# Optimization experiments

Hardware: AMD Instinct MI355X
Metric: run time of the kernel (lower is better)

## Reference

```python
import jax, jax.numpy as jnp
import numpy as np

N_NODES = 100000
N_EDGES = 1600000
N_GRAPHS = 100
DIMS = [128, 128, 118, 103, 5]  # in_feats, h, h-10, h-25, num_classes


def setup_inputs() -> dict:
    key = jax.random.key(0)
    ks = jax.random.split(key, 16)
    inp = {
        "in_feat": jax.random.normal(ks[0], (N_NODES, DIMS[0]), dtype=jnp.float32),
        "src": jax.random.randint(ks[1], (N_EDGES,), 0, N_NODES, dtype=jnp.int32),
        "dst": jax.random.randint(ks[2], (N_EDGES,), 0, N_NODES, dtype=jnp.int32),
        "graph_ids": (jnp.arange(N_NODES, dtype=jnp.int32) // (N_NODES // N_GRAPHS)),
    }
    # SAGEConv params: fc_self (no bias), fc_neigh (no bias), shared bias
    for l in range(4):
        din, dout = DIMS[l], DIMS[l + 1]
        inp[f"ws{l+1}"] = jax.random.normal(ks[3 + 3 * l], (din, dout), dtype=jnp.float32) * 0.05
        inp[f"wn{l+1}"] = jax.random.normal(ks[4 + 3 * l], (din, dout), dtype=jnp.float32) * 0.05
        inp[f"b{l+1}"] = jnp.zeros((dout,), dtype=jnp.float32)
    return inp


def reference(in_feat, src, dst, graph_ids,
              ws1, wn1, b1, ws2, wn2, b2, ws3, wn3, b3, ws4, wn4, b4):
    N = in_feat.shape[0]
    # in-degree per dst node, clamped to 1 (DGL: degs.clamp(min=1))
    deg = jnp.clip(jax.ops.segment_sum(jnp.ones((src.shape[0],), in_feat.dtype), dst,
                                       num_segments=N), 1.0, None)

    def sage(h, ws, wn, b):
        # mean-aggregate neighbor features: gather over src, scatter-add to dst
        agg = jax.ops.segment_sum(h[src], dst, num_segments=N) / deg[:, None]
        return h @ ws + agg @ wn + b

    h = jax.nn.relu(sage(in_feat, ws1, wn1, b1))
    h = jax.nn.relu(sage(h, ws2, wn2, b2))
    h = jax.nn.relu(sage(h, ws3, wn3, b3))
    h = sage(h, ws4, wn4, b4)

    # dgl.mean_nodes: per-graph mean pooling over nodes
    ones = jnp.ones((N,), h.dtype)
    cnt = jax.ops.segment_sum(ones, graph_ids, num_segments=N_GRAPHS)
    pooled = jax.ops.segment_sum(h, graph_ids, num_segments=N_GRAPHS) / cnt[:, None]
    return pooled
```

## Files before the change

kernel.cpp:

```cpp
#include <hip/hip_runtime.h>
#include <cstdint>
#include <cstddef>

typedef unsigned int uint32;
typedef unsigned short ushort16;
typedef __attribute__((ext_vector_type(8))) short short8;
typedef __attribute__((ext_vector_type(4))) float floatx4;

__device__ __forceinline__ ushort16 f2bf(float f) {
    uint32 u = __builtin_bit_cast(uint32, f);
    uint32 r = (u + 0x7fffu + ((u >> 16) & 1u)) >> 16;
    return (ushort16)r;
}
__device__ __forceinline__ float bf2f(ushort16 h) {
    uint32 u = ((uint32)h) << 16;
    return __builtin_bit_cast(float, u);
}

#define PBS 4096


__global__ __launch_bounds__(256) void bucket_hist_kernel(
    const int* __restrict__ dst, int* __restrict__ bcnt, int E, int NBUCK) {
    __shared__ int l[512];
    int t = threadIdx.x;
    for (int b = t; b < NBUCK; b += 256) l[b] = 0;
    __syncthreads();
    int e0 = blockIdx.x * PBS;
    int e1 = e0 + PBS; if (e1 > E) e1 = E;
    for (int j = e0 + t; j < e1; j += 256)
        atomicAdd(&l[dst[j] >> 8], 1);
    __syncthreads();
    for (int b = t; b < NBUCK; b += 256) {
        int c = l[b];
        if (c) atomicAdd(&bcnt[b], c);
    }
}

__global__ __launch_bounds__(256) void bucket_scan_kernel(
    const int* __restrict__ bcnt, int* __restrict__ bucketOff,
    int* __restrict__ cursorA, int NBUCK, int E) {
    __shared__ int a[512], b[512];
    int t = threadIdx.x;
    a[t] = (t < NBUCK) ? bcnt[t] : 0;
    a[t + 256] = (t + 256 < NBUCK) ? bcnt[t + 256] : 0;
    __syncthreads();
    int* cur = a; int* nxt = b;
    for (int o = 1; o < 512; o <<= 1) {
#pragma unroll
        for (int i = t; i < 512; i += 256)
            nxt[i] = cur[i] + ((i >= o) ? cur[i - o] : 0);
        __syncthreads();
        int* tmp = cur; cur = nxt; nxt = tmp;
    }
#pragma unroll
    for (int i = t; i < 512; i += 256) {
        if (i <= NBUCK) {
            int off = (i == 0) ? 0 : cur[i - 1];
            bucketOff[i] = off;
            if (i < NBUCK) cursorA[i] = off;
        }
    }
    if (t == 0) bucketOff[NBUCK] = E;
}

__global__ __launch_bounds__(256) void bucket_partition_kernel(
    const int* __restrict__ src, const int* __restrict__ dst,
    int* __restrict__ cursorA, uint32* __restrict__ ebuf, int E, int NBUCK) {
    __shared__ int lbase[512];
    int tid = threadIdx.x;
    for (int b = tid; b < NBUCK; b += 256) lbase[b] = 0;
    __syncthreads();
    int e0 = blockIdx.x * PBS;
    int e1 = e0 + PBS; if (e1 > E) e1 = E;
    for (int j = e0 + tid; j < e1; j += 256)
        atomicAdd(&lbase[dst[j] >> 8], 1);
    __syncthreads();
    for (int b = tid; b < NBUCK; b += 256) {
        int c = lbase[b];
        lbase[b] = c ? atomicAdd(&cursorA[b], c) : 0;
    }
    __syncthreads();
    for (int j = e0 + tid; j < e1; j += 256) {
        int d = dst[j];
        int p = atomicAdd(&lbase[d >> 8], 1);
        ebuf[p] = ((uint32)src[j] << 8) | (uint32)(d & 255);
    }
}

__global__ __launch_bounds__(256) void bucket_build_kernel(
    const uint32* __restrict__ ebuf, const int* __restrict__ bucketOff,
    int* __restrict__ row_ptr, float* __restrict__ degf,
    int* __restrict__ csr, int N, int E) {
    __shared__ int ldeg[256];
    __shared__ int lscan[256];
    __shared__ int lcur[256];
    int b = blockIdx.x, t = threadIdx.x;
    int n0 = b << 8;
    int s = bucketOff[b], e = bucketOff[b + 1];
    ldeg[t] = 0;
    __syncthreads();
    for (int j = s + t; j < e; j += 256)
        atomicAdd(&ldeg[ebuf[j] & 255u], 1);
    __syncthreads();
    int v = ldeg[t];
    lscan[t] = v;
    __syncthreads();
    for (int off = 1; off < 256; off <<= 1) {
        int x = (t >= off) ? lscan[t - off] : 0;
        __syncthreads();
        lscan[t] += x;
        __syncthreads();
    }
    int excl = lscan[t] - v;
    int node = n0 + t;
    if (node < N) {
        row_ptr[node] = s + excl;
        degf[node] = (float)(v > 0 ? v : 1);
    }
    lcur[t] = s + excl;
    __syncthreads();
    for (int j = s + t; j < e; j += 256) {
        uint32 en = ebuf[j];
        int p = atomicAdd(&lcur[en & 255u], 1);
        csr[p] = (int)(en >> 8);
    }
    if (b == 0 && t == 0) row_ptr[N] = E;
}

__global__ void conv_bf16_kernel(const float* __restrict__ x, ushort16* __restrict__ y, int n8) {
    int i = blockIdx.x * blockDim.x + threadIdx.x;
    if (i >= n8) return;
    const float4 a = *(const float4*)(x + (size_t)i * 8);
    const float4 b = *(const float4*)(x + (size_t)i * 8 + 4);
    uint4 o;
    o.x = (uint32)f2bf(a.x) | ((uint32)f2bf(a.y) << 16);
    o.y = (uint32)f2bf(a.z) | ((uint32)f2bf(a.w) << 16);
    o.z = (uint32)f2bf(b.x) | ((uint32)f2bf(b.y) << 16);
    o.w = (uint32)f2bf(b.z) | ((uint32)f2bf(b.w) << 16);
    *(uint4*)(y + (size_t)i * 8) = o;
}

__global__ void prep_w_all_kernel(
    const float* __restrict__ W0s, const float* __restrict__ W0n,
    const float* __restrict__ W1s, const float* __restrict__ W1n,
    const float* __restrict__ W2s, const float* __restrict__ W2n,
    ushort16* __restrict__ Whi, ushort16* __restrict__ Wlo) {
    int mat = blockIdx.x >> 6;
    int idx = (blockIdx.x & 63) * 256 + threadIdx.x;
    const float* Wt[6] = {W0s, W0n, W1s, W1n, W2s, W2n};
    const int Kt[6] = {128, 128, 128, 128, 118, 118};
    const int Mt[6] = {128, 128, 118, 118, 103, 103};
    int n = idx >> 7, k = idx & 127;
    int K = Kt[mat], M = Mt[mat];
    float w = (k < K && n < M) ? Wt[mat][(size_t)k * M + n] : 0.f;
    ushort16 h = f2bf(w);
    float lo = w - bf2f(h);
    Whi[(size_t)mat * 16384 + idx] = h;
    Wlo[(size_t)mat * 16384 + idx] = f2bf(lo);
}

template<int UNROLL>
__global__ __launch_bounds__(256) void aggregate_pre_kernel(
    const ushort16* __restrict__ h,
    const int* __restrict__ row_ptr, const int* __restrict__ csr,
    const float* __restrict__ degf, ushort16* __restrict__ aggH, int N) {
    int wid = threadIdx.x >> 6;
    int lane = threadIdx.x & 63;
    int node = blockIdx.x * 4 + wid;
    if (node >= N) return;
    int s = row_ptr[node], e = row_ptr[node + 1];
    int c = lane & 15;
    int eo = lane >> 4;
    float aLo[4] = {}, aHi[4] = {};
    int j = s + eo;
    for (; j + (UNROLL - 1) * 4 < e; j += UNROLL * 4) {
        uint4 v[UNROLL];
#pragma unroll
        for (int u = 0; u < UNROLL; ++u) {
            int src_n = csr[j + u * 4];
            v[u] = *(const uint4*)(h + ((size_t)src_n << 7) + (c << 3));
        }
#pragma unroll
        for (int u = 0; u < UNROLL; ++u) {
            uint32 w[4] = {v[u].x, v[u].y, v[u].z, v[u].w};
#pragma unroll
            for (int p = 0; p < 4; ++p) {
                aLo[p] += __builtin_bit_cast(float, w[p] << 16);
                aHi[p] += __builtin_bit_cast(float, w[p] & 0xffff0000u);
            }
        }
    }
    for (; j < e; j += 4) {
        int src_n = csr[j];
        uint4 v = *(const uint4*)(h + ((size_t)src_n << 7) + (c << 3));
        uint32 w[4] = {v.x, v.y, v.z, v.w};
#pragma unroll
        for (int p = 0; p < 4; ++p) {
            aLo[p] += __builtin_bit_cast(float, w[p] << 16);
            aHi[p] += __builtin_bit_cast(float, w[p] & 0xffff0000u);
        }
    }
#pragma unroll
    for (int m = 16; m < 64; m <<= 1) {
#pragma unroll
        for (int p = 0; p < 4; ++p) {
            aLo[p] += __shfl_xor(aLo[p], m, 64);
            aHi[p] += __shfl_xor(aHi[p], m, 64);
        }
    }
    if (lane < 16) {
        float inv = 1.f / degf[node];
        uint4 ov;
        ov.x = (uint32)f2bf(aLo[0] * inv) | ((uint32)f2bf(aHi[0] * inv) << 16);
        ov.y = (uint32)f2bf(aLo[1] * inv) | ((uint32)f2bf(aHi[1] * inv) << 16);
        ov.z = (uint32)f2bf(aLo[2] * inv) | ((uint32)f2bf(aHi[2] * inv) << 16);
        ov.w = (uint32)f2bf(aLo[3] * inv) | ((uint32)f2bf(aHi[3] * inv) << 16);
        *(uint4*)(aggH + ((size_t)node << 7) + (c << 3)) = ov;
    }
}

#define RS 40
__global__ __launch_bounds__(256) void mfma_fused_kernel(
    const ushort16* __restrict__ A, const ushort16* __restrict__ G,
    const ushort16* __restrict__ Whi, const ushort16* __restrict__ Wlo,
    const float* __restrict__ bias,
    ushort16* __restrict__ Out, int N, int M) {
    __shared__ ushort16 Bs[4][128 * RS];
    const int tid = threadIdx.x;
    const int wave = tid >> 6;
    const int lane = tid & 63;
    const int quad = lane >> 4;
    const int m16 = lane & 15;
    const ushort16* Wg[4] = {Whi, Wlo, Whi + 16384, Wlo + 16384};

    floatx4 acc[8] = {};

    int rowA = blockIdx.x * 64 + wave * 16 + m16;
    if (rowA >= N) rowA = N - 1;
    const ushort16* Arow = A + (size_t)rowA * 128;
    const ushort16* Grow = G + (size_t)rowA * 128;

    const int sn = tid >> 1, shalf = tid & 1;
    for (int k0 = 0; k0 < 128; k0 += 32) {
#pragma unroll
        for (int mat = 0; mat < 4; ++mat) {
            const ushort16* g = Wg[mat] + (size_t)sn * 128 + k0 + shalf * 16;
            uint4 v0 = *(const uint4*)(g);
            uint4 v1 = *(const uint4*)(g + 8);
            ushort16* d = &Bs[mat][sn * RS + shalf * 16];
            *(uint4*)(d) = v0;
            *(uint4*)(d + 8) = v1;
        }
        __syncthreads();
        short8 af = *(const short8*)(Arow + k0 + quad * 8);
        short8 gf = *(const short8*)(Grow + k0 + quad * 8);
#pragma unroll
        for (int t = 0; t < 8; ++t) {
            int nb = t * 16 + m16;
            short8 bsh = *(const short8*)(&Bs[0][nb * RS + quad * 8]);
            short8 bsl = *(const short8*)(&Bs[1][nb * RS + quad * 8]);
            short8 bnh = *(const short8*)(&Bs[2][nb * RS + quad * 8]);
            short8 bnl = *(const short8*)(&Bs[3][nb * RS + quad * 8]);
            acc[t] = __builtin_amdgcn_mfma_f32_16x16x32_bf16(af, bsh, acc[t], 0, 0, 0);
            acc[t] = __builtin_amdgcn_mfma_f32_16x16x32_bf16(gf, bnh, acc[t], 0, 0, 0);
            acc[t] = __builtin_amdgcn_mfma_f32_16x16x32_bf16(af, bsl, acc[t], 0, 0, 0);
            acc[t] = __builtin_amdgcn_mfma_f32_16x16x32_bf16(gf, bnl, acc[t], 0, 0, 0);
        }
        __syncthreads();
    }

    int rowBase = blockIdx.x * 64 + wave * 16 + quad * 4;
#pragma unroll
    for (int t = 0; t < 8; ++t) {
        int col = t * 16 + m16;
        bool inc = (col < M);
        float b = inc ? bias[col] : 0.f;
#pragma unroll
        for (int r = 0; r < 4; ++r) {
            int row = rowBase + r;
            if (row >= N) continue;
            float v = inc ? fmaxf(acc[t][r] + b, 0.f) : 0.f;
            Out[(size_t)row * 128 + col] = f2bf(v);
        }
    }
}

__global__ __launch_bounds__(256) void gemm4_kernel(
    const ushort16* __restrict__ A, const float* __restrict__ ws,
    const float* __restrict__ wn, const float* __restrict__ b4,
    float* __restrict__ Cs, float* __restrict__ Cn, int N, int K, int M) {
    __shared__ float Wsh[520], Wnh[520];
    int tid = threadIdx.x;
    for (int i = tid; i < K * M; i += 256) { Wsh[i] = ws[i]; Wnh[i] = wn[i]; }
    __syncthreads();
    int node = blockIdx.x * 256 + tid;
    if (node >= N) return;
    const ushort16* row = A + ((size_t)node << 7);
    float s[5] = {}, n[5] = {};
    for (int c8 = 0; c8 * 8 < K; ++c8) {
        uint4 v = *(const uint4*)(row + c8 * 8);
        uint32 w[4] = {v.x, v.y, v.z, v.w};
#pragma unroll
        for (int j = 0; j < 8; ++j) {
            int k = c8 * 8 + j;
            if (k < K) {
                float a = (j & 1) ? __builtin_bit_cast(float, w[j >> 1] & 0xffff0000u)
                                  : __builtin_bit_cast(float, w[j >> 1] << 16);
#pragma unroll
                for (int m = 0; m < 5; ++m) {
                    s[m] += a * Wsh[k * 5 + m];
                    n[m] += a * Wnh[k * 5 + m];
                }
            }
        }
    }
    size_t o = (size_t)node * 8;
#pragma unroll
    for (int m = 0; m < 5; ++m) {
        Cs[o + m] = s[m] + b4[m];
        Cn[o + m] = n[m];
    }
#pragma unroll
    for (int m = 5; m < 8; ++m) { Cs[o + m] = 0.f; Cn[o + m] = 0.f; }
}

template<int CPW, int UNROLL, int SLOG>
__global__ __launch_bounds__(256) void aggregate_fp32_kernel(
    const float* __restrict__ hs, const float* __restrict__ hn,
    const int* __restrict__ row_ptr, const int* __restrict__ csr,
    const float* __restrict__ degf, float* __restrict__ out, int N) {
    constexpr int EPI = 64 / CPW;
    int wid = threadIdx.x >> 6;
    int lane = threadIdx.x & 63;
    int node = blockIdx.x * 4 + wid;
    if (node >= N) return;
    int s = row_ptr[node], e = row_ptr[node + 1];
    int c = lane & (CPW - 1);
    int eo = lane / CPW;
    float4 acc = make_float4(0.f, 0.f, 0.f, 0.f);
    int j = s + eo;
    for (; j + (UNROLL - 1) * EPI < e; j += UNROLL * EPI) {
        float4 v[UNROLL];
#pragma unroll
        for (int u = 0; u < UNROLL; ++u) {
            int src_n = csr[j + u * EPI];
            v[u] = *(const float4*)(hn + ((size_t)src_n << SLOG) + (c << 2));
        }
#pragma unroll
        for (int u = 0; u < UNROLL; ++u) {
            acc.x += v[u].x; acc.y += v[u].y; acc.z += v[u].z; acc.w += v[u].w;
        }
    }
    for (; j < e; j += EPI) {
        int src_n = csr[j];
        float4 v = *(const float4*)(hn + ((size_t)src_n << SLOG) + (c << 2));
        acc.x += v.x; acc.y += v.y; acc.z += v.z; acc.w += v.w;
    }
#pragma unroll
    for (int m = CPW; m < 64; m <<= 1) {
        acc.x += __shfl_xor(acc.x, m, 64);
        acc.y += __shfl_xor(acc.y, m, 64);
        acc.z += __shfl_xor(acc.z, m, 64);
        acc.w += __shfl_xor(acc.w, m, 64);
    }
    if (lane < CPW) {
        float d = 1.f / degf[node];
        size_t o = ((size_t)node << SLOG) + (lane << 2);
        float4 hv = *(const float4*)(hs + o);
        float4 r;
        r.x = hv.x + acc.x * d;
        r.y = hv.y + acc.y * d;
        r.z = hv.z + acc.z * d;
        r.w = hv.w + acc.w * d;
        *(float4*)(out + o) = r;
    }
}

__global__ __launch_bounds__(256) void pool_kernel(
    const float* __restrict__ h, float* __restrict__ out, int npg) {
    __shared__ float sh[4][5];
    int g = blockIdx.x;
    int t = threadIdx.x;
    float acc[5] = {0.f, 0.f, 0.f, 0.f, 0.f};
    int base = g * npg;
    for (int i = t; i < npg; i += 256) {
        const float* r = h + ((size_t)(base + i) << 3);
#pragma unroll
        for (int f = 0; f < 5; ++f) acc[f] += r[f];
    }
#pragma unroll
    for (int off = 32; off > 0; off >>= 1) {
#pragma unroll
        for (int f = 0; f < 5; ++f) acc[f] += __shfl_down(acc[f], off, 64);
    }
    int wid = t >> 6, lane = t & 63;
    if (lane == 0) {
#pragma unroll
        for (int f = 0; f < 5; ++f) sh[wid][f] = acc[f];
    }
    __syncthreads();
    if (t == 0) {
        float inv = 1.f / (float)npg;
#pragma unroll
        for (int f = 0; f < 5; ++f)
            out[g * 5 + f] = (sh[0][f] + sh[1][f] + sh[2][f] + sh[3][f]) * inv;
    }
}

extern "C" void kernel_launch(void* const* d_in, const int* in_sizes, int n_in,
                              void* d_out, int out_size, void* d_ws, size_t ws_size,
                              hipStream_t stream) {
    const float* in_feat = (const float*)d_in[0];
    const int* src = (const int*)d_in[1];
    const int* dst = (const int*)d_in[2];
    const int DIMS[5] = {128, 128, 118, 103, 5};
    const int N = in_sizes[0] / 128;
    const int E = in_sizes[1];
    const int G = out_size / 5;
    const int NBUCK = (N + 255) >> 8;

    char* base = (char*)d_ws;
    size_t off = 0;
    auto carve = [&](size_t bytes) -> void* {
        off = (off + 255) & ~(size_t)255;
        void* p = base + off;
        off += bytes;
        return p;
    };
    int* bcnt = (int*)carve((size_t)NBUCK * 4);
    int* bucketOff = (int*)carve((size_t)(NBUCK + 1) * 4);
    int* cursorA = (int*)carve((size_t)NBUCK * 4);
    int* row_ptr = (int*)carve((size_t)(N + 1) * 4);
    float* degf = (float*)carve((size_t)N * 4);
    uint32* ebuf = (uint32*)carve((size_t)E * 4);
    int* csr = (int*)carve((size_t)E * 4);
    ushort16* buf0 = (ushort16*)carve((size_t)(N + 64) * 128 * 2);
    ushort16* buf1 = (ushort16*)carve((size_t)(N + 64) * 128 * 2);
    ushort16* aggH = (ushort16*)carve((size_t)(N + 64) * 128 * 2);
    ushort16* Whi = (ushort16*)carve((size_t)6 * 16384 * 2);
    ushort16* Wlo = (ushort16*)carve((size_t)6 * 16384 * 2);
    float* Cs4 = (float*)carve((size_t)N * 8 * 4);
    float* Cn4 = (float*)carve((size_t)N * 8 * 4);
    float* out4 = (float*)carve((size_t)N * 8 * 4);
    (void)n_in; (void)ws_size;

    hipMemsetAsync(bcnt, 0, (size_t)NBUCK * 4, stream);
    bucket_hist_kernel<<<(E + PBS - 1) / PBS, 256, 0, stream>>>(dst, bcnt, E, NBUCK);
    bucket_scan_kernel<<<1, 256, 0, stream>>>(bcnt, bucketOff, cursorA, NBUCK, E);
    bucket_partition_kernel<<<(E + PBS - 1) / PBS, 256, 0, stream>>>(
        src, dst, cursorA, ebuf, E, NBUCK);
    bucket_build_kernel<<<NBUCK, 256, 0, stream>>>(
        ebuf, bucketOff, row_ptr, degf, csr, N, E);

    int n8 = N * 16;
    conv_bf16_kernel<<<(n8 + 255) / 256, 256, 0, stream>>>(in_feat, buf0, n8);
    prep_w_all_kernel<<<6 * 64, 256, 0, stream>>>(
        (const float*)d_in[4], (const float*)d_in[5],
        (const float*)d_in[7], (const float*)d_in[8],
        (const float*)d_in[10], (const float*)d_in[11],
        Whi, Wlo);

    ushort16* hb[4] = {buf0, buf1, buf0, buf1};
    int gblocks = (N + 63) / 64;
    for (int l = 0; l < 3; ++l) {
        int M = DIMS[l + 1];
        const float* b = (const float*)d_in[6 + 3 * l];
        aggregate_pre_kernel<4><<<(N + 3) / 4, 256, 0, stream>>>(
            hb[l], row_ptr, csr, degf, aggH, N);
        mfma_fused_kernel<<<gblocks, 256, 0, stream>>>(
            hb[l], aggH, Whi + (size_t)l * 2 * 16384, Wlo + (size_t)l * 2 * 16384,
            b, hb[l + 1], N, M);
    }

    gemm4_kernel<<<(N + 255) / 256, 256, 0, stream>>>(
        hb[3], (const float*)d_in[13], (const float*)d_in[14], (const float*)d_in[15],
        Cs4, Cn4, N, DIMS[3], DIMS[4]);
    aggregate_fp32_kernel<2, 1, 3><<<(N + 3) / 4, 256, 0, stream>>>(
        Cs4, Cn4, row_ptr, csr, degf, out4, N);
    pool_kernel<<<G, 256, 0, stream>>>(out4, (float*)d_out, N / G);
}
```

Baseline: 520.2 us.

## Drop LDS weight staging and tile 64 rows per wave in fused MFMA GEMM

Restructures the fused layer GEMM so each wave keeps a 64-row tile of A and aggregated features in registers, and reads weight fragments straight from global memory (L2-cached) instead of staging them in shared memory behind barriers. Each weight fragment is now reused across four row sub-tiles, which removes the __syncthreads and the LDS traffic. Each block now covers 256 rows, so there are fewer blocks. The cost is much higher register pressure (32 short8 input fragments held per lane), which lowers occupancy, plus uncoalesced global weight loads.

```diff
diff --git a/kernel.cpp b/kernel.cpp
--- a/kernel.cpp
+++ b/kernel.cpp
@@ -18,7 +18,6 @@
 }
 
 #define PBS 4096
-
 
 __global__ __launch_bounds__(256) void bucket_hist_kernel(
     const int* __restrict__ dst, int* __restrict__ bcnt, int E, int NBUCK) {
@@ -220,68 +219,70 @@
     }
 }
 
-#define RS 40
 __global__ __launch_bounds__(256) void mfma_fused_kernel(
     const ushort16* __restrict__ A, const ushort16* __restrict__ G,
     const ushort16* __restrict__ Whi, const ushort16* __restrict__ Wlo,
     const float* __restrict__ bias,
     ushort16* __restrict__ Out, int N, int M) {
-    __shared__ ushort16 Bs[4][128 * RS];
     const int tid = threadIdx.x;
     const int wave = tid >> 6;
     const int lane = tid & 63;
     const int quad = lane >> 4;
     const int m16 = lane & 15;
-    const ushort16* Wg[4] = {Whi, Wlo, Whi + 16384, Wlo + 16384};
-
-    floatx4 acc[8] = {};
-
-    int rowA = blockIdx.x * 64 + wave * 16 + m16;
-    if (rowA >= N) rowA = N - 1;
-    const ushort16* Arow = A + (size_t)rowA * 128;
-    const ushort16* Grow = G + (size_t)rowA * 128;
-
-    const int sn = tid >> 1, shalf = tid & 1;
-    for (int k0 = 0; k0 < 128; k0 += 32) {
-#pragma unroll
-        for (int mat = 0; mat < 4; ++mat) {
-            const ushort16* g = Wg[mat] + (size_t)sn * 128 + k0 + shalf * 16;
-            uint4 v0 = *(const uint4*)(g);
-            uint4 v1 = *(const uint4*)(g + 8);
-            ushort16* d = &Bs[mat][sn * RS + shalf * 16];
-            *(uint4*)(d) = v0;
-            *(uint4*)(d + 8) = v1;
-        }
-        __syncthreads();
-        short8 af = *(const short8*)(Arow + k0 + quad * 8);
-        short8 gf = *(const short8*)(Grow + k0 + quad * 8);
-#pragma unroll
-        for (int t = 0; t < 8; ++t) {
-            int nb = t * 16 + m16;
-            short8 bsh = *(const short8*)(&Bs[0][nb * RS + quad * 8]);
-            short8 bsl = *(const short8*)(&Bs[1][nb * RS + quad * 8]);
-            short8 bnh = *(const short8*)(&Bs[2][nb * RS + quad * 8]);
-            short8 bnl = *(const short8*)(&Bs[3][nb * RS + quad * 8]);
-            acc[t] = __builtin_amdgcn_mfma_f32_16x16x32_bf16(af, bsh, acc[t], 0, 0, 0);
-            acc[t] = __builtin_amdgcn_mfma_f32_16x16x32_bf16(gf, bnh, acc[t], 0, 0, 0);
-            acc[t] = __builtin_amdgcn_mfma_f32_16x16x32_bf16(af, bsl, acc[t], 0, 0, 0);
-            acc[t] = __builtin_amdgcn_mfma_f32_16x16x32_bf16(gf, bnl, acc[t], 0, 0, 0);
-        }
-        __syncthreads();
-    }
-
-    int rowBase = blockIdx.x * 64 + wave * 16 + quad * 4;
+    const ushort16* Ws_hi = Whi;
+    const ushort16* Ws_lo = Wlo;
+    const ushort16* Wn_hi = Whi + 16384;
+    const ushort16* Wn_lo = Wlo + 16384;
+
+    const int tilebase = (blockIdx.x * 4 + wave) * 64;
+
+    short8 af[4][4], gf[4][4];
+#pragma unroll
+    for (int i = 0; i < 4; ++i) {
+        int row = tilebase + i * 16 + m16;
+        if (row >= N) row = N - 1;
+        const ushort16* Ar = A + (size_t)row * 128 + quad * 8;
+        const ushort16* Gr = G + (size_t)row * 128 + quad * 8;
+#pragma unroll
+        for (int k = 0; k < 4; ++k) {
+            af[i][k] = *(const short8*)(Ar + k * 32);
+            gf[i][k] = *(const short8*)(Gr + k * 32);
+        }
+    }
+
 #pragma unroll
     for (int t = 0; t < 8; ++t) {
-        int col = t * 16 + m16;
-        bool inc = (col < M);
-        float b = inc ? bias[col] : 0.f;
-#pragma unroll
-        for (int r = 0; r < 4; ++r) {
-            int row = rowBase + r;
-            if (row >= N) continue;
-            float v = inc ? fmaxf(acc[t][r] + b, 0.f) : 0.f;
-            Out[(size_t)row * 128 + col] = f2bf(v);
+        floatx4 acc[4] = {};
+        const int nb = t * 16 + m16;
+        const size_t boff = (size_t)nb * 128 + quad * 8;
+#pragma unroll
+        for (int k = 0; k < 4; ++k) {
+            short8 bsh = *(const short8*)(Ws_hi + boff + k * 32);
+            short8 bnh = *(const short8*)(Wn_hi + boff + k * 32);
+            short8 bsl = *(const short8*)(Ws_lo + boff + k * 32);
+            short8 bnl = *(const short8*)(Wn_lo + boff + k * 32);
+#pragma unroll
+            for (int i = 0; i < 4; ++i) {
+                acc[i] = __builtin_amdgcn_mfma_f32_16x16x32_bf16(af[i][k], bsh, acc[i], 0, 0, 0);
+                acc[i] = __builtin_amdgcn_mfma_f32_16x16x32_bf16(gf[i][k], bnh, acc[i], 0, 0, 0);
+                acc[i] = __builtin_amdgcn_mfma_f32_16x16x32_bf16(af[i][k], bsl, acc[i], 0, 0, 0);
+                acc[i] = __builtin_amdgcn_mfma_f32_16x16x32_bf16(gf[i][k], bnl, acc[i], 0, 0, 0);
+            }
+        }
+        const int colt = t * 16 + m16;
+        const bool inc = (colt < M);
+        const float b = inc ? bias[colt] : 0.f;
+#pragma unroll
+        for (int i = 0; i < 4; ++i) {
+            int rowBase = tilebase + i * 16 + quad * 4;
+#pragma unroll
+            for (int r = 0; r < 4; ++r) {
+                int row = rowBase + r;
+                if (row < N) {
+                    float v = inc ? fmaxf(acc[i][r] + b, 0.f) : 0.f;
+                    Out[(size_t)row * 128 + colt] = f2bf(v);
+                }
+            }
         }
     }
 }
@@ -435,9 +436,9 @@
     float* degf = (float*)carve((size_t)N * 4);
     uint32* ebuf = (uint32*)carve((size_t)E * 4);
     int* csr = (int*)carve((size_t)E * 4);
-    ushort16* buf0 = (ushort16*)carve((size_t)(N + 64) * 128 * 2);
-    ushort16* buf1 = (ushort16*)carve((size_t)(N + 64) * 128 * 2);
-    ushort16* aggH = (ushort16*)carve((size_t)(N + 64) * 128 * 2);
+    ushort16* buf0 = (ushort16*)carve((size_t)(N + 256) * 128 * 2);
+    ushort16* buf1 = (ushort16*)carve((size_t)(N + 256) * 128 * 2);
+    ushort16* aggH = (ushort16*)carve((size_t)(N + 256) * 128 * 2);
     ushort16* Whi = (ushort16*)carve((size_t)6 * 16384 * 2);
     ushort16* Wlo = (ushort16*)carve((size_t)6 * 16384 * 2);
     float* Cs4 = (float*)carve((size_t)N * 8 * 4);
@@ -462,7 +463,7 @@
         Whi, Wlo);
 
     ushort16* hb[4] = {buf0, buf1, buf0, buf1};
-    int gblocks = (N + 63) / 64;
+    int gblocks = (N + 255) / 256;
     for (int l = 0; l < 3; ++l) {
         int M = DIMS[l + 1];
         const float* b = (const float*)d_in[6 + 3 * l];
```

Result: slower. 564.2 us (+8.5%).

## Fuse neighbor aggregation into the MFMA layer GEMM via LDS

Applied to the files above, without the earlier changes.

Merges the per-layer mean-aggregation kernel into the MFMA GEMM kernel. Each 64-row block first gathers and averages neighbor features for its rows into shared memory, then runs the dual-weight bf16 MFMA using the LDS aggregate instead of a global aggH buffer. This removes one launch per layer and the global write and read of the aggregated features. In exchange, only 4 waves per block do the gather, 16 nodes each in sequence, so latency hiding may drop, and the extra LDS cuts occupancy. A third ping-pong buffer is added so a layer never reads and writes the same buffer.

```diff
diff --git a/kernel.cpp b/kernel.cpp
--- a/kernel.cpp
+++ b/kernel.cpp
@@ -18,7 +18,6 @@
 }
 
 #define PBS 4096
-
 
 __global__ __launch_bounds__(256) void bucket_hist_kernel(
     const int* __restrict__ dst, int* __restrict__ bcnt, int E, int NBUCK) {
@@ -160,86 +159,88 @@
     Wlo[(size_t)mat * 16384 + idx] = f2bf(lo);
 }
 
-template<int UNROLL>
-__global__ __launch_bounds__(256) void aggregate_pre_kernel(
-    const ushort16* __restrict__ h,
+#define RS 40
+#define GHS 136
+__global__ __launch_bounds__(256) void layer_fused_kernel(
+    const ushort16* __restrict__ A,
     const int* __restrict__ row_ptr, const int* __restrict__ csr,
-    const float* __restrict__ degf, ushort16* __restrict__ aggH, int N) {
-    int wid = threadIdx.x >> 6;
-    int lane = threadIdx.x & 63;
-    int node = blockIdx.x * 4 + wid;
-    if (node >= N) return;
-    int s = row_ptr[node], e = row_ptr[node + 1];
-    int c = lane & 15;
-    int eo = lane >> 4;
-    float aLo[4] = {}, aHi[4] = {};
-    int j = s + eo;
-    for (; j + (UNROLL - 1) * 4 < e; j += UNROLL * 4) {
-        uint4 v[UNROLL];
-#pragma unroll
-        for (int u = 0; u < UNROLL; ++u) {
-            int src_n = csr[j + u * 4];
-            v[u] = *(const uint4*)(h + ((size_t)src_n << 7) + (c << 3));
-        }
-#pragma unroll
-        for (int u = 0; u < UNROLL; ++u) {
-            uint32 w[4] = {v[u].x, v[u].y, v[u].z, v[u].w};
-#pragma unroll
-            for (int p = 0; p < 4; ++p) {
-                aLo[p] += __builtin_bit_cast(float, w[p] << 16);
-                aHi[p] += __builtin_bit_cast(float, w[p] & 0xffff0000u);
-            }
-        }
-    }
-    for (; j < e; j += 4) {
-        int src_n = csr[j];
-        uint4 v = *(const uint4*)(h + ((size_t)src_n << 7) + (c << 3));
-        uint32 w[4] = {v.x, v.y, v.z, v.w};
-#pragma unroll
-        for (int p = 0; p < 4; ++p) {
-            aLo[p] += __builtin_bit_cast(float, w[p] << 16);
-            aHi[p] += __builtin_bit_cast(float, w[p] & 0xffff0000u);
-        }
-    }
-#pragma unroll
-    for (int m = 16; m < 64; m <<= 1) {
-#pragma unroll
-        for (int p = 0; p < 4; ++p) {
-            aLo[p] += __shfl_xor(aLo[p], m, 64);
-            aHi[p] += __shfl_xor(aHi[p], m, 64);
-        }
-    }
-    if (lane < 16) {
-        float inv = 1.f / degf[node];
-        uint4 ov;
-        ov.x = (uint32)f2bf(aLo[0] * inv) | ((uint32)f2bf(aHi[0] * inv) << 16);
-        ov.y = (uint32)f2bf(aLo[1] * inv) | ((uint32)f2bf(aHi[1] * inv) << 16);
-        ov.z = (uint32)f2bf(aLo[2] * inv) | ((uint32)f2bf(aHi[2] * inv) << 16);
-        ov.w = (uint32)f2bf(aLo[3] * inv) | ((uint32)f2bf(aHi[3] * inv) << 16);
-        *(uint4*)(aggH + ((size_t)node << 7) + (c << 3)) = ov;
-    }
-}
-
-#define RS 40
-__global__ __launch_bounds__(256) void mfma_fused_kernel(
-    const ushort16* __restrict__ A, const ushort16* __restrict__ G,
+    const float* __restrict__ degf,
     const ushort16* __restrict__ Whi, const ushort16* __restrict__ Wlo,
     const float* __restrict__ bias,
     ushort16* __restrict__ Out, int N, int M) {
     __shared__ ushort16 Bs[4][128 * RS];
+    __shared__ ushort16 Gs[64 * GHS];
     const int tid = threadIdx.x;
     const int wave = tid >> 6;
     const int lane = tid & 63;
     const int quad = lane >> 4;
     const int m16 = lane & 15;
+    const int blockbase = blockIdx.x * 64;
+
+    {
+        const int c = lane & 15;
+        const int eo = lane >> 4;
+        for (int i = 0; i < 16; ++i) {
+            int lrow = wave * 16 + i;
+            int node = blockbase + lrow;
+            if (node >= N) break;
+            int s = row_ptr[node], e = row_ptr[node + 1];
+            float aLo[4] = {}, aHi[4] = {};
+            int j = s + eo;
+            for (; j + 12 < e; j += 16) {
+                uint4 v[4];
+#pragma unroll
+                for (int u = 0; u < 4; ++u) {
+                    int src_n = csr[j + u * 4];
+                    v[u] = *(const uint4*)(A + ((size_t)src_n << 7) + (c << 3));
+                }
+#pragma unroll
+                for (int u = 0; u < 4; ++u) {
+                    uint32 w[4] = {v[u].x, v[u].y, v[u].z, v[u].w};
+#pragma unroll
+                    for (int p = 0; p < 4; ++p) {
+                        aLo[p] += __builtin_bit_cast(float, w[p] << 16);
+                        aHi[p] += __builtin_bit_cast(float, w[p] & 0xffff0000u);
+                    }
+                }
+            }
+            for (; j < e; j += 4) {
+                int src_n = csr[j];
+                uint4 v = *(const uint4*)(A + ((size_t)src_n << 7) + (c << 3));
+                uint32 w[4] = {v.x, v.y, v.z, v.w};
+#pragma unroll
+                for (int p = 0; p < 4; ++p) {
+                    aLo[p] += __builtin_bit_cast(float, w[p] << 16);
+                    aHi[p] += __builtin_bit_cast(float, w[p] & 0xffff0000u);
+                }
+            }
+#pragma unroll
+            for (int m = 16; m < 64; m <<= 1) {
+#pragma unroll
+                for (int p = 0; p < 4; ++p) {
+                    aLo[p] += __shfl_xor(aLo[p], m, 64);
+                    aHi[p] += __shfl_xor(aHi[p], m, 64);
+                }
+            }
+            if (lane < 16) {
+                float inv = 1.f / degf[node];
+                uint4 ov;
+                ov.x = (uint32)f2bf(aLo[0] * inv) | ((uint32)f2bf(aHi[0] * inv) << 16);
+                ov.y = (uint32)f2bf(aLo[1] * inv) | ((uint32)f2bf(aHi[1] * inv) << 16);
+                ov.z = (uint32)f2bf(aLo[2] * inv) | ((uint32)f2bf(aHi[2] * inv) << 16);
+                ov.w = (uint32)f2bf(aLo[3] * inv) | ((uint32)f2bf(aHi[3] * inv) << 16);
+                *(uint4*)(&Gs[lrow * GHS + (c << 3)]) = ov;
+            }
+        }
+    }
+    __syncthreads();
+
     const ushort16* Wg[4] = {Whi, Wlo, Whi + 16384, Wlo + 16384};
-
     floatx4 acc[8] = {};
-
-    int rowA = blockIdx.x * 64 + wave * 16 + m16;
+    int rowA = blockbase + wave * 16 + m16;
     if (rowA >= N) rowA = N - 1;
     const ushort16* Arow = A + (size_t)rowA * 128;
-    const ushort16* Grow = G + (size_t)rowA * 128;
+    const ushort16* Glds = Gs + (wave * 16 + m16) * GHS;
 
     const int sn = tid >> 1, shalf = tid & 1;
     for (int k0 = 0; k0 < 128; k0 += 32) {
@@ -252,9 +253,9 @@
             *(uint4*)(d) = v0;
             *(uint4*)(d + 8) = v1;
         }
+        short8 af = *(const short8*)(Arow + k0 + quad * 8);
         __syncthreads();
-        short8 af = *(const short8*)(Arow + k0 + quad * 8);
-        short8 gf = *(const short8*)(Grow + k0 + quad * 8);
+        short8 gf = *(const short8*)(Glds + k0 + quad * 8);
 #pragma unroll
         for (int t = 0; t < 8; ++t) {
             int nb = t * 16 + m16;
@@ -270,18 +271,19 @@
         __syncthreads();
     }
 
-    int rowBase = blockIdx.x * 64 + wave * 16 + quad * 4;
+    int rowBase = blockbase + wave * 16 + quad * 4;
 #pragma unroll
     for (int t = 0; t < 8; ++t) {
-        int col = t * 16 + m16;
-        bool inc = (col < M);
-        float b = inc ? bias[col] : 0.f;
+        int colt = t * 16 + m16;
+        bool inc = (colt < M);
+        float b = inc ? bias[colt] : 0.f;
 #pragma unroll
         for (int r = 0; r < 4; ++r) {
             int row = rowBase + r;
-            if (row >= N) continue;
-            float v = inc ? fmaxf(acc[t][r] + b, 0.f) : 0.f;
-            Out[(size_t)row * 128 + col] = f2bf(v);
+            if (row < N) {
+                float v = inc ? fmaxf(acc[t][r] + b, 0.f) : 0.f;
+                Out[(size_t)row * 128 + colt] = f2bf(v);
+            }
         }
     }
 }
@@ -435,9 +437,9 @@
     float* degf = (float*)carve((size_t)N * 4);
     uint32* ebuf = (uint32*)carve((size_t)E * 4);
     int* csr = (int*)carve((size_t)E * 4);
-    ushort16* buf0 = (ushort16*)carve((size_t)(N + 64) * 128 * 2);
-    ushort16* buf1 = (ushort16*)carve((size_t)(N + 64) * 128 * 2);
-    ushort16* aggH = (ushort16*)carve((size_t)(N + 64) * 128 * 2);
+    ushort16* buf0 = (ushort16*)carve((size_t)(N + 256) * 128 * 2);
+    ushort16* buf1 = (ushort16*)carve((size_t)(N + 256) * 128 * 2);
+    ushort16* buf2 = (ushort16*)carve((size_t)(N + 256) * 128 * 2);
     ushort16* Whi = (ushort16*)carve((size_t)6 * 16384 * 2);
     ushort16* Wlo = (ushort16*)carve((size_t)6 * 16384 * 2);
     float* Cs4 = (float*)carve((size_t)N * 8 * 4);
@@ -461,15 +463,14 @@
         (const float*)d_in[10], (const float*)d_in[11],
         Whi, Wlo);
 
-    ushort16* hb[4] = {buf0, buf1, buf0, buf1};
+    ushort16* hb[4] = {buf0, buf1, buf2, buf0};
     int gblocks = (N + 63) / 64;
     for (int l = 0; l < 3; ++l) {
         int M = DIMS[l + 1];
         const float* b = (const float*)d_in[6 + 3 * l];
-        aggregate_pre_kernel<4><<<(N + 3) / 4, 256, 0, stream>>>(
-            hb[l], row_ptr, csr, degf, aggH, N);
-        mfma_fused_kernel<<<gblocks, 256, 0, stream>>>(
-            hb[l], aggH, Whi + (size_t)l * 2 * 16384, Wlo + (size_t)l * 2 * 16384,
+        layer_fused_kernel<<<gblocks, 256, 0, stream>>>(
+            hb[l], row_ptr, csr, degf,
+            Whi + (size_t)l * 2 * 16384, Wlo + (size_t)l * 2 * 16384,
             b, hb[l + 1], N, M);
     }
 
```

Result: slower. 847.4 us (+62.9%).
